# Kernel tuning notes

Measured on AMD Instinct MI355X. Metric: run time of the kernel, lower is better.

Reference implementation:

```python
import jax, jax.numpy as jnp
import numpy as np

HEADS = (4, 2, 1)
OUTS = (32, 16, 2)
NEG_SLOPE = 0.2


def gat_conv(x, src, dst, W, att_s, att_d, b, heads, out_dim, n_nodes, concat):
    # x: [N, Fin] -> h: [N, H, Fout]
    h = (x @ W).reshape(n_nodes, heads, out_dim)
    # per-node attention terms, gathered to edges: [E, H]
    a_src = jnp.sum(h * att_s, axis=-1)
    a_dst = jnp.sum(h * att_d, axis=-1)
    logits = jax.nn.leaky_relu(a_src[src] + a_dst[dst], NEG_SLOPE)
    # segment softmax over incoming edges of each destination node
    lmax = jax.ops.segment_max(logits, dst, num_segments=n_nodes)[dst]
    e = jnp.exp(logits - lmax)
    denom = jax.ops.segment_sum(e, dst, num_segments=n_nodes)[dst]
    alpha = e / denom  # [E, H]
    # weighted message aggregation
    msg = h[src] * alpha[:, :, None]  # [E, H, Fout]
    agg = jax.ops.segment_sum(msg, dst, num_segments=n_nodes)  # [N, H, Fout]
    if concat:
        agg = agg.reshape(n_nodes, heads * out_dim)
    else:
        agg = agg.mean(axis=1)
    return agg + b


def _glorot(key, shape):
    fan = shape[0] + shape[-1] if len(shape) == 2 else shape[-1] * 2
    s = jnp.sqrt(6.0 / fan)
    return jax.random.uniform(key, shape, jnp.float32, -s, s)


def setup_inputs() -> dict:
    key = jax.random.key(0)
    N, E, FIN = 100000, 1600000, 128
    ks = jax.random.split(key, 16)
    x = jax.random.normal(ks[0], (N, FIN), jnp.float32)
    edge_index = jax.random.randint(ks[1], (2, E), 0, N, jnp.int64)
    ins = (FIN, HEADS[0] * OUTS[0], HEADS[1] * OUTS[1])
    d = {"x": x, "edge_index": edge_index}
    for i in range(3):
        H, O = HEADS[i], OUTS[i]
        d[f"W{i+1}"] = _glorot(ks[2 + 4 * i], (ins[i], H * O))
        d[f"att_s{i+1}"] = _glorot(ks[3 + 4 * i], (H, O))
        d[f"att_d{i+1}"] = _glorot(ks[4 + 4 * i], (H, O))
        bdim = H * O if i < 2 else O
        d[f"b{i+1}"] = jnp.zeros((bdim,), jnp.float32)
    return d


def reference(x, edge_index, W1, att_s1, att_d1, b1, W2, att_s2, att_d2, b2, W3, att_s3, att_d3, b3):
    N = x.shape[0]
    loops = jnp.arange(N, dtype=edge_index.dtype)
    src = jnp.concatenate([edge_index[0], loops])
    dst = jnp.concatenate([edge_index[1], loops])
    h = gat_conv(x, src, dst, W1, att_s1, att_d1, b1, HEADS[0], OUTS[0], N, True)
    h = jax.nn.elu(h)
    h = gat_conv(h, src, dst, W2, att_s2, att_d2, b2, HEADS[1], OUTS[1], N, True)
    h = jax.nn.elu(h)
    h = gat_conv(h, src, dst, W3, att_s3, att_d3, b3, HEADS[2], OUTS[2], N, False)
    return jax.nn.log_softmax(h, axis=1)
```

## Files before the change

kernel.cpp:

```cpp
#include <hip/hip_runtime.h>
#include <math.h>

static __device__ __forceinline__ float lrelu(float x){ return fmaxf(x, 0.2f*x); }
static __device__ __forceinline__ float eluf(float x){ return x > 0.f ? x : __expf(x)-1.f; }
static __device__ __forceinline__ float fexp2(float x){ return __builtin_amdgcn_exp2f(x); }
static __device__ __forceinline__ unsigned short f2bf(float f){
  unsigned int u = __float_as_uint(f);
  unsigned int r = (u + 0x7FFFu + ((u>>16)&1u)) >> 16;
  return (unsigned short)r;
}
static __device__ __forceinline__ float bflo(unsigned int u){ return __uint_as_float(u<<16); }
static __device__ __forceinline__ float bfhi(unsigned int u){ return __uint_as_float(u & 0xFFFF0000u); }

#define LOG2E 1.44269504f
#define CLAMP2 115.41f
#define ECAP 4096

typedef __attribute__((ext_vector_type(8))) short short8;
typedef __attribute__((ext_vector_type(4))) float f32x4;

static __device__ __forceinline__ uint4 ld16(const uint4* base, unsigned eoff){
  return *(const uint4*)((const char*)base + (size_t)(eoff*16u));
}
static __device__ __forceinline__ float ldf(const float* base, unsigned eoff){
  return *(const float*)((const char*)base + (size_t)(eoff*4u));
}

#define DETECT_IS64(ei_, s_is64_) \
  if (threadIdx.x < 64){ \
    int w_ = ((const int*)(ei_))[2*threadIdx.x + 1]; \
    unsigned long long b_ = __ballot(w_ != 0); \
    if (threadIdx.x == 0) s_is64_ = (b_ == 0ull); \
  } \
  __syncthreads();

__global__ void k_wprep(const float* __restrict__ W1, const float* __restrict__ W2,
                        unsigned short* __restrict__ wf1, unsigned short* __restrict__ wf2,
                        int* __restrict__ gcnt, int NB){
  int e = blockIdx.x*256 + threadIdx.x;
  if (e < NB) gcnt[e] = 0;
  if (e < 2048){
    int lane = e&63, ct = (e>>6)&7, ks = e>>9;
    int q = lane>>4, n = lane&15;
    union { unsigned short us[8]; uint4 u; } pk;
    #pragma unroll
    for (int j=0;j<8;j++)
      pk.us[j] = f2bf(W1[(ks*32 + q*8 + j)*128 + ct*16 + n]);
    *(uint4*)&wf1[(size_t)e*8] = pk.u;
  } else if (e < 2048+512){
    int e2 = e - 2048;
    int lane = e2&63, ct = (e2>>6)&1, ks = e2>>7;
    int q = lane>>4, n = lane&15;
    union { unsigned short us[8]; uint4 u; } pk;
    #pragma unroll
    for (int j=0;j<8;j++)
      pk.us[j] = f2bf(W2[(ks*32 + q*8 + j)*32 + ct*16 + n]);
    *(uint4*)&wf2[(size_t)e2*8] = pk.u;
  }
}

#define BS_ITEMS 16
__global__ __launch_bounds__(256) void k_scat_gemm1(
    const void* __restrict__ ei, int* __restrict__ gcnt,
    unsigned int* __restrict__ ebuf, int E, int NB, int GS,
    const float* __restrict__ x, const unsigned short* __restrict__ wf,
    const float* __restrict__ atts, const float* __restrict__ attd,
    unsigned short* __restrict__ hb, float* __restrict__ as_, float* __restrict__ ad_,
    int N){
  __shared__ __align__(16) unsigned char smem[50176];
  __shared__ int s_is64;
  int t = threadIdx.x;
  if ((int)blockIdx.x < GS){
    int* lcnt  = (int*)smem;
    int* lbase = lcnt + NB;
    for (int i=t; i<NB; i+=256) lcnt[i]=0;
    DETECT_IS64(ei, s_is64)
    bool is64 = s_is64 != 0;
    int base = blockIdx.x*(256*BS_ITEMS);
    unsigned int ent[BS_ITEMS]; int bk[BS_ITEMS]; int lofs[BS_ITEMS];
    #pragma unroll
    for (int i=0;i<BS_ITEMS;i++){
      int e = base + i*256 + t;
      if (e < E){
        int s, d;
        if (is64){ const long long* p=(const long long*)ei; s=(int)p[e]; d=(int)p[(size_t)E+e]; }
        else     { const int* p=(const int*)ei;            s=p[e];      d=p[(size_t)E+e]; }
        int b = d>>7;
        bk[i] = b;
        ent[i] = (unsigned int)s | ((unsigned int)(d & 127) << 25);
        lofs[i] = atomicAdd(&lcnt[b], 1);
      } else bk[i] = -1;
    }
    __syncthreads();
    for (int i=t; i<NB; i+=256){
      int c = lcnt[i];
      lbase[i] = c ? atomicAdd(&gcnt[i], c) : 0;
    }
    __syncthreads();
    #pragma unroll
    for (int i=0;i<BS_ITEMS;i++){
      if (bk[i] >= 0){
        int pos = lbase[bk[i]] + lofs[i];
        if (pos < ECAP)
          ebuf[(size_t)bk[i]*ECAP + pos] = ent[i];
      }
    }
  } else {
    unsigned short* xs  = (unsigned short*)smem;
    unsigned short* wsm = (unsigned short*)(smem + 64*136*2);
    int r0 = ((int)blockIdx.x - GS)*64;
    {
      const uint4* src = (const uint4*)wf;
      uint4* dst = (uint4*)wsm;
      #pragma unroll
      for (int i=0;i<8;i++) dst[t + i*256] = src[t + i*256];
    }
    {
      #pragma unroll
      for (int i=0;i<4;i++){
        int idx = t + i*256;
        int row = idx>>4, k8 = (idx&15)*8;
        int gr = r0 + row;
        float4 v0 = make_float4(0.f,0.f,0.f,0.f), v1 = v0;
        if (gr < N){
          v0 = *(const float4*)&x[(size_t)gr*128 + k8];
          v1 = *(const float4*)&x[(size_t)gr*128 + k8 + 4];
        }
        union { unsigned short us[8]; uint4 u; } pk;
        pk.us[0]=f2bf(v0.x); pk.us[1]=f2bf(v0.y); pk.us[2]=f2bf(v0.z); pk.us[3]=f2bf(v0.w);
        pk.us[4]=f2bf(v1.x); pk.us[5]=f2bf(v1.y); pk.us[6]=f2bf(v1.z); pk.us[7]=f2bf(v1.w);
        *(uint4*)&xs[row*136 + k8] = pk.u;
      }
    }
    __syncthreads();
    int w = t>>6, lane = t&63, lm = lane&15, q = lane>>4;
    int rt0 = (w&1)*2;
    int ct0 = (w>>1)*4;
    f32x4 acc[2][4];
    #pragma unroll
    for (int a=0;a<2;a++)
      #pragma unroll
      for (int c=0;c<4;c++) acc[a][c] = (f32x4){0.f,0.f,0.f,0.f};
    #pragma unroll
    for (int ks=0;ks<4;ks++){
      short8 a0 = *(const short8*)&xs[( rt0   *16 + lm)*136 + ks*32 + q*8];
      short8 a1 = *(const short8*)&xs[((rt0+1)*16 + lm)*136 + ks*32 + q*8];
      #pragma unroll
      for (int c=0;c<4;c++){
        short8 b = *(const short8*)&wsm[((ks*8 + ct0 + c)*64 + lane)*8];
        acc[0][c] = __builtin_amdgcn_mfma_f32_16x16x32_bf16(a0, b, acc[0][c], 0,0,0);
        acc[1][c] = __builtin_amdgcn_mfma_f32_16x16x32_bf16(a1, b, acc[1][c], 0,0,0);
      }
    }
    __syncthreads();
    #pragma unroll
    for (int rl=0;rl<2;rl++)
      #pragma unroll
      for (int c=0;c<4;c++)
        #pragma unroll
        for (int r=0;r<4;r++)
          xs[((rt0+rl)*16 + q*4 + r)*136 + (ct0+c)*16 + lm] = f2bf(acc[rl][c][r]);
    __syncthreads();
    {
      #pragma unroll
      for (int i=0;i<4;i++){
        int idx = t + i*256;
        int row = idx>>4, c8 = (idx&15)*8;
        int gr = r0 + row;
        if (gr < N)
          *(uint4*)&hb[(size_t)gr*128 + c8] = *(const uint4*)&xs[row*136 + c8];
      }
    }
    {
      int row = t>>2, h = t&3;
      int gr = r0 + row;
      if (gr < N){
        const unsigned short* hr = &xs[row*136 + h*32];
        const float* sa = atts + h*32;
        const float* da = attd + h*32;
        float ss = 0.f, dd = 0.f;
        #pragma unroll
        for (int o=0;o<32;o+=8){
          uint4 v = *(const uint4*)&hr[o];
          float hv[8] = { bflo(v.x),bfhi(v.x),bflo(v.y),bfhi(v.y),
                          bflo(v.z),bfhi(v.z),bflo(v.w),bfhi(v.w) };
          #pragma unroll
          for (int m=0;m<8;m++){ ss += hv[m]*sa[o+m]; dd += hv[m]*da[o+m]; }
        }
        as_[gr*4+h] = ss*LOG2E; ad_[gr*4+h] = dd*LOG2E;
      }
    }
  }
}

__global__ __launch_bounds__(256) void k_bcsr(const unsigned int* __restrict__ ebuf,
    const int* __restrict__ gcnt,
    int* __restrict__ rp, int* __restrict__ re, int* __restrict__ csr, int N, int NB){
  __shared__ unsigned int lde[ECAP];
  __shared__ unsigned short lofp[ECAP];
  __shared__ int lcnt[128];
  __shared__ int lexc[128];
  __shared__ int sc[256];
  int b = blockIdx.x, t = threadIdx.x;
  int d0 = b<<7;
  int R = N - d0; if (R > 128) R = 128;
  if (t < 128) lcnt[t]=0;
  __syncthreads();
  size_t base = (size_t)b*ECAP;
  int cnt = gcnt[b]; if (cnt > ECAP) cnt = ECAP;
  for (int i=t; i<cnt; i+=256){
    unsigned int e = ebuf[base+i];
    lde[i] = e;
    lofp[i] = (unsigned short)atomicAdd(&lcnt[e>>25], 1);
  }
  __syncthreads();
  int v = (t<128)? lcnt[t] : 0;
  sc[t]=v; __syncthreads();
  for (int off=1; off<128; off<<=1){
    int add = (t>=off)? sc[t-off] : 0;
    __syncthreads();
    sc[t]+=add;
    __syncthreads();
  }
  if (t<128) lexc[t] = sc[t]-v;
  __syncthreads();
  if (t < R){
    int s = (int)base + lexc[t];
    rp[d0+t] = s;
    re[d0+t] = s + lcnt[t];
  }
  for (int i=t; i<cnt; i+=256){
    unsigned int e = lde[i];
    csr[base + lexc[e>>25] + lofp[i]] = (int)(e & 0x1FFFFFFu);
  }
}

__global__ __launch_bounds__(256) void k_mgemm2(const unsigned short* __restrict__ xb,
    const unsigned short* __restrict__ wf,
    const float* __restrict__ atts, const float* __restrict__ attd,
    unsigned short* __restrict__ hb2, float* __restrict__ as_, float* __restrict__ ad_,
    int N){
  __shared__ unsigned short xs[128*136];
  __shared__ unsigned short wsm[512*8];
  int t = threadIdx.x;
  int r0 = blockIdx.x*128;
  {
    #pragma unroll
    for (int i=0;i<2;i++)
      ((uint4*)wsm)[t + i*256] = ((const uint4*)wf)[t + i*256];
  }
  {
    #pragma unroll
    for (int i=0;i<8;i++){
      int idx = t + i*256;
      int row = idx>>4, c8 = (idx&15)*8;
      int gr = r0 + row;
      uint4 v = make_uint4(0u,0u,0u,0u);
      if (gr < N) v = *(const uint4*)&xb[(size_t)gr*128 + c8];
      *(uint4*)&xs[row*136 + c8] = v;
    }
  }
  __syncthreads();
  int w = t>>6, lane = t&63, lm = lane&15, q = lane>>4;
  int rt0 = 2*w;
  f32x4 acc[2][2];
  #pragma unroll
  for (int a=0;a<2;a++){ acc[a][0] = (f32x4){0.f,0.f,0.f,0.f}; acc[a][1] = acc[a][0]; }
  #pragma unroll
  for (int ks=0;ks<4;ks++){
    short8 a0 = *(const short8*)&xs[( rt0   *16 + lm)*136 + ks*32 + q*8];
    short8 a1 = *(const short8*)&xs[((rt0+1)*16 + lm)*136 + ks*32 + q*8];
    #pragma unroll
    for (int c=0;c<2;c++){
      short8 b = *(const short8*)&wsm[((ks*2 + c)*64 + lane)*8];
      acc[0][c] = __builtin_amdgcn_mfma_f32_16x16x32_bf16(a0, b, acc[0][c], 0,0,0);
      acc[1][c] = __builtin_amdgcn_mfma_f32_16x16x32_bf16(a1, b, acc[1][c], 0,0,0);
    }
  }
  __syncthreads();
  #pragma unroll
  for (int rl=0;rl<2;rl++)
    #pragma unroll
    for (int c=0;c<2;c++)
      #pragma unroll
      for (int r=0;r<4;r++)
        xs[((rt0+rl)*16 + q*4 + r)*136 + c*16 + lm] = f2bf(acc[rl][c][r]);
  __syncthreads();
  {
    #pragma unroll
    for (int i=0;i<2;i++){
      int idx = t + i*256;
      int row = idx>>2, c8 = (idx&3)*8;
      int gr = r0 + row;
      if (gr < N)
        *(uint4*)&hb2[(size_t)gr*32 + c8] = *(const uint4*)&xs[row*136 + c8];
    }
  }
  {
    int row = t>>1, h = t&1;
    int gr = r0 + row;
    if (gr < N){
      const unsigned short* hr = &xs[row*136 + h*16];
      const float* sa = atts + h*16;
      const float* da = attd + h*16;
      float ss = 0.f, dd = 0.f;
      #pragma unroll
      for (int o=0;o<16;o+=8){
        uint4 v = *(const uint4*)&hr[o];
        float hv[8] = { bflo(v.x),bfhi(v.x),bflo(v.y),bfhi(v.y),
                        bflo(v.z),bfhi(v.z),bflo(v.w),bfhi(v.w) };
        #pragma unroll
        for (int m=0;m<8;m++){ ss += hv[m]*sa[o+m]; dd += hv[m]*da[o+m]; }
      }
      as_[gr*2+h] = ss*LOG2E; ad_[gr*2+h] = dd*LOG2E;
    }
  }
}

#define ACC8(v_, w_) { \
  a[0]+=w_*bflo(v_.x); a[1]+=w_*bfhi(v_.x); a[2]+=w_*bflo(v_.y); a[3]+=w_*bfhi(v_.y); \
  a[4]+=w_*bflo(v_.z); a[5]+=w_*bfhi(v_.z); a[6]+=w_*bflo(v_.w); a[7]+=w_*bfhi(v_.w); }

__global__ __launch_bounds__(256) void k_agg1(const int* __restrict__ rp, const int* __restrict__ re,
    const int* __restrict__ csr,
    const float* __restrict__ as_, const float* __restrict__ ad_,
    const uint4* __restrict__ hb4, const float* __restrict__ bias,
    unsigned short* __restrict__ outb, int n0, int nlim){
  int n = n0 + blockIdx.x*16 + (threadIdx.x>>4);
  if (n >= nlim) return;
  int li = threadIdx.x & 15, ghead = li>>2;
  int start = rp[n], end = re[n];
  float adh = ldf(ad_, (unsigned)n*4u+ghead);
  float a[8];
  #pragma unroll
  for (int k=0;k<8;k++) a[k]=0.f;
  float wse = fexp2(fminf(lrelu(ldf(as_, (unsigned)n*4u+ghead) + adh), CLAMP2));
  float l = wse;
  { uint4 v = ld16(hb4, (unsigned)n*16u + li); ACC8(v, wse) }
  int i = start;
  for (; i + 1 < end; i += 2){
    int s0 = csr[i];
    int s1 = csr[i+1];
    float w0 = fexp2(fminf(lrelu(ldf(as_, (unsigned)s0*4u+ghead) + adh), CLAMP2));
    float w1 = fexp2(fminf(lrelu(ldf(as_, (unsigned)s1*4u+ghead) + adh), CLAMP2));
    uint4 v0 = ld16(hb4, (unsigned)s0*16u + li);
    uint4 v1 = ld16(hb4, (unsigned)s1*16u + li);
    l += w0 + w1;
    ACC8(v0, w0)
    ACC8(v1, w1)
  }
  if (i < end){
    int s = csr[i];
    float w = fexp2(fminf(lrelu(ldf(as_, (unsigned)s*4u+ghead) + adh), CLAMP2));
    uint4 v = ld16(hb4, (unsigned)s*16u + li);
    l += w;
    ACC8(v, w)
  }
  float invh = 1.f/l;
  float4 b0 = *(const float4*)&bias[li*8];
  float4 b1 = *(const float4*)&bias[li*8+4];
  union { unsigned short us[8]; uint4 v; } pk;
  pk.us[0]=f2bf(eluf(a[0]*invh+b0.x)); pk.us[1]=f2bf(eluf(a[1]*invh+b0.y));
  pk.us[2]=f2bf(eluf(a[2]*invh+b0.z)); pk.us[3]=f2bf(eluf(a[3]*invh+b0.w));
  pk.us[4]=f2bf(eluf(a[4]*invh+b1.x)); pk.us[5]=f2bf(eluf(a[5]*invh+b1.y));
  pk.us[6]=f2bf(eluf(a[6]*invh+b1.z)); pk.us[7]=f2bf(eluf(a[7]*invh+b1.w));
  *(uint4*)&outb[(size_t)n*128 + li*8] = pk.v;
}

__global__ __launch_bounds__(256) void k_agg2(const int* __restrict__ rp, const int* __restrict__ re,
    const int* __restrict__ csr,
    const float* __restrict__ as_, const float* __restrict__ ad_,
    const uint4* __restrict__ hb4, const float* __restrict__ bias,
    const float* __restrict__ W3, const float* __restrict__ atts3,
    const float* __restrict__ attd3,
    float4* __restrict__ pk4, int N){
  int n = blockIdx.x*64 + (threadIdx.x>>2);
  if (n >= N) return;
  int li = threadIdx.x & 3, ghead = li>>1;
  int start = rp[n], end = re[n];
  float adh = ldf(ad_, (unsigned)n*2u+ghead);
  float a[8];
  #pragma unroll
  for (int k=0;k<8;k++) a[k]=0.f;
  float wse = fexp2(fminf(lrelu(ldf(as_, (unsigned)n*2u+ghead) + adh), CLAMP2));
  float l = wse;
  { uint4 v = ld16(hb4, (unsigned)n*4u + li); ACC8(v, wse) }
  int i = start;
  for (; i + 1 < end; i += 2){
    int s0 = csr[i];
    int s1 = csr[i+1];
    float w0 = fexp2(fminf(lrelu(ldf(as_, (unsigned)s0*2u+ghead) + adh), CLAMP2));
    float w1 = fexp2(fminf(lrelu(ldf(as_, (unsigned)s1*2u+ghead) + adh), CLAMP2));
    uint4 v0 = ld16(hb4, (unsigned)s0*4u + li);
    uint4 v1 = ld16(hb4, (unsigned)s1*4u + li);
    l += w0 + w1;
    ACC8(v0, w0)
    ACC8(v1, w1)
  }
  if (i < end){
    int s = csr[i];
    float w = fexp2(fminf(lrelu(ldf(as_, (unsigned)s*2u+ghead) + adh), CLAMP2));
    uint4 v = ld16(hb4, (unsigned)s*4u + li);
    l += w;
    ACC8(v, w)
  }
  float invh = 1.f/l;
  float r0_ = eluf(a[0]*invh + bias[li*8+0]);
  float r1_ = eluf(a[1]*invh + bias[li*8+1]);
  float r2_ = eluf(a[2]*invh + bias[li*8+2]);
  float r3_ = eluf(a[3]*invh + bias[li*8+3]);
  float r4_ = eluf(a[4]*invh + bias[li*8+4]);
  float r5_ = eluf(a[5]*invh + bias[li*8+5]);
  float r6_ = eluf(a[6]*invh + bias[li*8+6]);
  float r7_ = eluf(a[7]*invh + bias[li*8+7]);
  const float* wr = &W3[li*16];
  float p0 = r0_*wr[0] + r1_*wr[2] + r2_*wr[4]  + r3_*wr[6]
           + r4_*wr[8] + r5_*wr[10]+ r6_*wr[12] + r7_*wr[14];
  float p1 = r0_*wr[1] + r1_*wr[3] + r2_*wr[5]  + r3_*wr[7]
           + r4_*wr[9] + r5_*wr[11]+ r6_*wr[13] + r7_*wr[15];
  p0 += __shfl_xor(p0,1); p0 += __shfl_xor(p0,2);
  p1 += __shfl_xor(p1,1); p1 += __shfl_xor(p1,2);
  if (li == 0){
    float4 pk;
    pk.x = p0; pk.y = p1;
    pk.z = (p0*atts3[0] + p1*atts3[1])*LOG2E;
    pk.w = (p0*attd3[0] + p1*attd3[1])*LOG2E;
    pk4[n] = pk;
  }
}

__global__ __launch_bounds__(256) void k_agg3(const int* __restrict__ rp, const int* __restrict__ re,
    const int* __restrict__ csr,
    const float4* __restrict__ pk4, const float* __restrict__ bias,
    float* __restrict__ out, int N){
  int n = blockIdx.x*16 + (threadIdx.x>>4);
  if (n >= N) return;
  int li = threadIdx.x & 15;
  int start = rp[n], end = re[n];
  float4 self = pk4[n];
  float adh = self.w;
  float l = 0.f;
  float2 acc = make_float2(0.f, 0.f);
  for (int i=start+li; i<end; i+=16){
    int s = csr[i];
    float4 ps = pk4[s];
    float w = fexp2(fminf(lrelu(ps.z + adh), CLAMP2));
    l += w;
    acc.x += w*ps.x; acc.y += w*ps.y;
  }
  if (li == 0){
    float w = fexp2(fminf(lrelu(self.z + adh), CLAMP2));
    l += w;
    acc.x += w*self.x; acc.y += w*self.y;
  }
  #pragma unroll
  for (int msk=1; msk<16; msk<<=1){
    l += __shfl_xor(l, msk);
    acc.x += __shfl_xor(acc.x, msk);
    acc.y += __shfl_xor(acc.y, msk);
  }
  if (li == 0){
    float inv = 1.f/l;
    float g0 = acc.x*inv + bias[0];
    float g1 = acc.y*inv + bias[1];
    float mm = fmaxf(g0, g1);
    float lse = mm + logf(__expf(g0-mm) + __expf(g1-mm));
    *(float2*)&out[2*n] = make_float2(g0-lse, g1-lse);
  }
}

extern "C" void kernel_launch(void* const* d_in, const int* in_sizes, int n_in,
                              void* d_out, int out_size, void* d_ws, size_t ws_size,
                              hipStream_t stream) {
  const float* x   = (const float*)d_in[0];
  const void*  ei  = d_in[1];
  const float* W1  = (const float*)d_in[2];
  const float* as1 = (const float*)d_in[3];
  const float* ad1 = (const float*)d_in[4];
  const float* b1  = (const float*)d_in[5];
  const float* W2  = (const float*)d_in[6];
  const float* as2 = (const float*)d_in[7];
  const float* ad2 = (const float*)d_in[8];
  const float* b2  = (const float*)d_in[9];
  const float* W3  = (const float*)d_in[10];
  const float* as3 = (const float*)d_in[11];
  const float* ad3 = (const float*)d_in[12];
  const float* b3  = (const float*)d_in[13];

  int N = in_sizes[0] / 128;
  int E = in_sizes[1] / 2;
  int NB = (N + 127) >> 7;

  char* w = (char*)d_ws;
  size_t off = 0;
  auto alloc = [&](size_t bytes)->void*{
    void* p = w + off; off += (bytes + 255) & ~(size_t)255; return p;
  };
  int*   gcnt    = (int*)alloc((size_t)NB*4);
  int*   rp      = (int*)alloc((size_t)N*4);
  int*   re      = (int*)alloc((size_t)N*4);
  unsigned int* ebuf = (unsigned int*)alloc((size_t)NB*ECAP*4);
  int*   csr     = (int*)alloc((size_t)NB*ECAP*4);
  float* as_buf  = (float*)alloc((size_t)N*4*4);
  float* ad_buf  = (float*)alloc((size_t)N*4*4);
  unsigned short* wf1 = (unsigned short*)alloc(2048*8*2);
  unsigned short* wf2 = (unsigned short*)alloc(512*8*2);
  unsigned short* hb  = (unsigned short*)alloc((size_t)N*128*2);
  unsigned short* xb  = (unsigned short*)alloc((size_t)N*128*2);
  unsigned short* hb2 = (unsigned short*)alloc((size_t)N*32*2);
  float4* pk4    = (float4*)alloc((size_t)N*16);
  if (off > ws_size) return;

  k_wprep<<<10, 256, 0, stream>>>(W1, W2, wf1, wf2, gcnt, NB);

  int GS = (E + 256*BS_ITEMS - 1) / (256*BS_ITEMS);
  int G1 = (N + 63)/64;
  k_scat_gemm1<<<GS + G1, 256, 0, stream>>>(ei, gcnt, ebuf, E, NB, GS,
                                            x, wf1, as1, ad1, hb, as_buf, ad_buf, N);
  k_bcsr<<<NB, 256, 0, stream>>>(ebuf, gcnt, rp, re, csr, N, NB);

  int Nh = ((N >> 1) + 15) & ~15;
  if (Nh > N) Nh = N;
  k_agg1<<<(Nh + 15)/16, 256, 0, stream>>>(rp, re, csr, as_buf, ad_buf,
                                           (const uint4*)hb, b1, xb, 0, Nh);
  if (N > Nh)
    k_agg1<<<(N - Nh + 15)/16, 256, 0, stream>>>(rp, re, csr, as_buf, ad_buf,
                                                 (const uint4*)hb, b1, xb, Nh, N);

  k_mgemm2<<<(N + 127)/128, 256, 0, stream>>>(xb, wf2, as2, ad2, hb2, as_buf, ad_buf, N);
  k_agg2<<<(N + 63)/64, 256, 0, stream>>>(rp, re, csr, as_buf, ad_buf, (const uint4*)hb2, b2,
                                          W3, as3, ad3, pk4, N);

  k_agg3<<<(N + 15)/16, 256, 0, stream>>>(rp, re, csr, pk4, b3, (float*)d_out, N);
}
```

Before: 296.8 us.

## Load GEMM1 A-fragments directly to registers, shrink LDS, merge agg1 launches

The GEMM half of the fused scatter/GEMM1 kernel now converts x rows to bf16 straight into MFMA A-fragment registers instead of staging them in LDS, and the LDS array shrinks from about 49KB to 32KB (reused for the output tile). It adds a launch-bounds occupancy hint of 4 blocks per CU. This aims to raise occupancy and remove one LDS round trip and barrier. The two half-range k_agg1 launches are merged into one, saving a launch. Register pressure from holding 8 short8 fragments may rise, and each lane now does narrower, less coalesced global reads of x.

Result: faster. 290.1 us (median of 2 runs) (-2.3%).

```diff
diff --git a/kernel.cpp b/kernel.cpp
--- a/kernel.cpp
+++ b/kernel.cpp
@@ -60,14 +60,14 @@
 }
 
 #define BS_ITEMS 16
-__global__ __launch_bounds__(256) void k_scat_gemm1(
+__global__ __launch_bounds__(256, 4) void k_scat_gemm1(
     const void* __restrict__ ei, int* __restrict__ gcnt,
     unsigned int* __restrict__ ebuf, int E, int NB, int GS,
     const float* __restrict__ x, const unsigned short* __restrict__ wf,
     const float* __restrict__ atts, const float* __restrict__ attd,
     unsigned short* __restrict__ hb, float* __restrict__ as_, float* __restrict__ ad_,
     int N){
-  __shared__ __align__(16) unsigned char smem[50176];
+  __shared__ __align__(16) unsigned char smem[32768];
   __shared__ int s_is64;
   int t = threadIdx.x;
   if ((int)blockIdx.x < GS){
@@ -106,8 +106,7 @@
       }
     }
   } else {
-    unsigned short* xs  = (unsigned short*)smem;
-    unsigned short* wsm = (unsigned short*)(smem + 64*136*2);
+    unsigned short* wsm = (unsigned short*)smem;
     int r0 = ((int)blockIdx.x - GS)*64;
     {
       const uint4* src = (const uint4*)wf;
@@ -115,27 +114,29 @@
       #pragma unroll
       for (int i=0;i<8;i++) dst[t + i*256] = src[t + i*256];
     }
-    {
-      #pragma unroll
-      for (int i=0;i<4;i++){
-        int idx = t + i*256;
-        int row = idx>>4, k8 = (idx&15)*8;
-        int gr = r0 + row;
-        float4 v0 = make_float4(0.f,0.f,0.f,0.f), v1 = v0;
-        if (gr < N){
-          v0 = *(const float4*)&x[(size_t)gr*128 + k8];
-          v1 = *(const float4*)&x[(size_t)gr*128 + k8 + 4];
-        }
-        union { unsigned short us[8]; uint4 u; } pk;
-        pk.us[0]=f2bf(v0.x); pk.us[1]=f2bf(v0.y); pk.us[2]=f2bf(v0.z); pk.us[3]=f2bf(v0.w);
-        pk.us[4]=f2bf(v1.x); pk.us[5]=f2bf(v1.y); pk.us[6]=f2bf(v1.z); pk.us[7]=f2bf(v1.w);
-        *(uint4*)&xs[row*136 + k8] = pk.u;
-      }
-    }
-    __syncthreads();
     int w = t>>6, lane = t&63, lm = lane&15, q = lane>>4;
     int rt0 = (w&1)*2;
     int ct0 = (w>>1)*4;
+    short8 af[2][4];
+    #pragma unroll
+    for (int rl=0; rl<2; rl++){
+      int gr = r0 + (rt0+rl)*16 + lm;
+      bool ok = gr < N;
+      const float* xr = &x[(size_t)(ok ? gr : 0)*128];
+      #pragma unroll
+      for (int ks=0; ks<4; ks++){
+        float4 v0 = make_float4(0.f,0.f,0.f,0.f), v1 = v0;
+        if (ok){
+          v0 = *(const float4*)&xr[ks*32 + q*8];
+          v1 = *(const float4*)&xr[ks*32 + q*8 + 4];
+        }
+        union { unsigned short us[8]; short8 s8; } pk;
+        pk.us[0]=f2bf(v0.x); pk.us[1]=f2bf(v0.y); pk.us[2]=f2bf(v0.z); pk.us[3]=f2bf(v0.w);
+        pk.us[4]=f2bf(v1.x); pk.us[5]=f2bf(v1.y); pk.us[6]=f2bf(v1.z); pk.us[7]=f2bf(v1.w);
+        af[rl][ks] = pk.s8;
+      }
+    }
+    __syncthreads();
     f32x4 acc[2][4];
     #pragma unroll
     for (int a=0;a<2;a++)
@@ -143,16 +144,15 @@
       for (int c=0;c<4;c++) acc[a][c] = (f32x4){0.f,0.f,0.f,0.f};
     #pragma unroll
     for (int ks=0;ks<4;ks++){
-      short8 a0 = *(const short8*)&xs[( rt0   *16 + lm)*136 + ks*32 + q*8];
-      short8 a1 = *(const short8*)&xs[((rt0+1)*16 + lm)*136 + ks*32 + q*8];
       #pragma unroll
       for (int c=0;c<4;c++){
         short8 b = *(const short8*)&wsm[((ks*8 + ct0 + c)*64 + lane)*8];
-        acc[0][c] = __builtin_amdgcn_mfma_f32_16x16x32_bf16(a0, b, acc[0][c], 0,0,0);
-        acc[1][c] = __builtin_amdgcn_mfma_f32_16x16x32_bf16(a1, b, acc[1][c], 0,0,0);
+        acc[0][c] = __builtin_amdgcn_mfma_f32_16x16x32_bf16(af[0][ks], b, acc[0][c], 0,0,0);
+        acc[1][c] = __builtin_amdgcn_mfma_f32_16x16x32_bf16(af[1][ks], b, acc[1][c], 0,0,0);
       }
     }
     __syncthreads();
+    unsigned short* xs = wsm;
     #pragma unroll
     for (int rl=0;rl<2;rl++)
       #pragma unroll
@@ -325,9 +325,9 @@
     const int* __restrict__ csr,
     const float* __restrict__ as_, const float* __restrict__ ad_,
     const uint4* __restrict__ hb4, const float* __restrict__ bias,
-    unsigned short* __restrict__ outb, int n0, int nlim){
-  int n = n0 + blockIdx.x*16 + (threadIdx.x>>4);
-  if (n >= nlim) return;
+    unsigned short* __restrict__ outb, int N){
+  int n = blockIdx.x*16 + (threadIdx.x>>4);
+  if (n >= N) return;
   int li = threadIdx.x & 15, ghead = li>>2;
   int start = rp[n], end = re[n];
   float adh = ldf(ad_, (unsigned)n*4u+ghead);
@@ -519,13 +519,7 @@
                                             x, wf1, as1, ad1, hb, as_buf, ad_buf, N);
   k_bcsr<<<NB, 256, 0, stream>>>(ebuf, gcnt, rp, re, csr, N, NB);
 
-  int Nh = ((N >> 1) + 15) & ~15;
-  if (Nh > N) Nh = N;
-  k_agg1<<<(Nh + 15)/16, 256, 0, stream>>>(rp, re, csr, as_buf, ad_buf,
-                                           (const uint4*)hb, b1, xb, 0, Nh);
-  if (N > Nh)
-    k_agg1<<<(N - Nh + 15)/16, 256, 0, stream>>>(rp, re, csr, as_buf, ad_buf,
-                                                 (const uint4*)hb, b1, xb, Nh, N);
+  k_agg1<<<(N + 15)/16, 256, 0, stream>>>(rp, re, csr, as_buf, ad_buf, (const uint4*)hb, b1, xb, N);
 
   k_mgemm2<<<(N + 127)/128, 256, 0, stream>>>(xb, wf2, as2, ad2, hb2, as_buf, ad_buf, N);
   k_agg2<<<(N + 63)/64, 256, 0, stream>>>(rp, re, csr, as_buf, ad_buf, (const uint4*)hb2, b2,
```
